# Kernel tuning notes

Hardware: AMD Instinct MI355X
Metric: run time of the kernel (lower is better)

The kernel has to match this reference:

```python
import jax, jax.numpy as jnp
import numpy as np

EPS = 1e-5  # torch BatchNorm1d default eps


def _bn(x, g, b, m, v):
    # x: [B, C, L]; params: [C] (inference-mode BN using running stats)
    scale = g / jnp.sqrt(v + EPS)
    return x * scale[None, :, None] + (b - m * scale)[None, :, None]


def setup_inputs() -> dict:
    key = jax.random.key(0)
    ks = jax.random.split(key, 16)
    B, C, L, I = 32, 256, 4096, 64
    d = {
        "x_a": jax.random.normal(ks[0], (B, C, L), jnp.float32),
        "x_b": jax.random.normal(ks[1], (B, C, L), jnp.float32),
        "x_c": jax.random.normal(ks[2], (B, C, L), jnp.float32),
        "w1": jax.random.normal(ks[3], (4, I, C), jnp.float32) * 0.05,
        "b1": jax.random.normal(ks[4], (4, I), jnp.float32) * 0.05,
        "bn1_g": jax.random.uniform(ks[5], (4, I), jnp.float32, 0.5, 1.5),
        "bn1_b": jax.random.normal(ks[6], (4, I), jnp.float32) * 0.05,
        "bn1_m": jax.random.normal(ks[7], (4, I), jnp.float32) * 0.05,
        "bn1_v": jax.random.uniform(ks[8], (4, I), jnp.float32, 0.5, 1.5),
        "w2": jax.random.normal(ks[9], (4, C, I), jnp.float32) * 0.05,
        "b2": jax.random.normal(ks[10], (4, C), jnp.float32) * 0.05,
        "bn2_g": jax.random.uniform(ks[11], (4, C), jnp.float32, 0.5, 1.5),
        "bn2_b": jax.random.normal(ks[12], (4, C), jnp.float32) * 0.05,
        "bn2_m": jax.random.normal(ks[13], (4, C), jnp.float32) * 0.05,
        "bn2_v": jax.random.uniform(ks[14], (4, C), jnp.float32, 0.5, 1.5),
    }
    return d


def reference(x_a, x_b, x_c, w1, b1, bn1_g, bn1_b, bn1_m, bn1_v,
              w2, b2, bn2_g, bn2_b, bn2_m, bn2_v):
    def att(x, i, global_pool):
        # branch i: conv1x1 -> BN -> ReLU -> conv1x1 -> BN
        h = jnp.mean(x, axis=-1, keepdims=True) if global_pool else x
        h = jnp.einsum('bcl,ic->bil', h, w1[i]) + b1[i][None, :, None]
        h = jax.nn.relu(_bn(h, bn1_g[i], bn1_b[i], bn1_m[i], bn1_v[i]))
        h = jnp.einsum('bil,ci->bcl', h, w2[i]) + b2[i][None, :, None]
        return _bn(h, bn2_g[i], bn2_b[i], bn2_m[i], bn2_v[i])

    x_ab = x_a + x_b
    wei = jax.nn.sigmoid(att(x_ab, 0, False) + att(x_ab, 1, True))  # [B,C,L]
    xo1 = x_a * wei + x_b * (1.0 - wei)

    x_abc = xo1 + x_c
    wei2 = jax.nn.sigmoid(att(x_abc, 2, False) + att(x_abc, 3, True))
    # NOTE: faithful to source: second blend uses (1 - wei), not (1 - wei2)
    xo2 = xo1 * wei2 + x_c * (1.0 - wei)
    return (xo1 + xo2) * 0.5
```

## Files before the change

kernel.cpp:

```cpp
#include <hip/hip_runtime.h>
#include <cstddef>

#define EPS_ 1e-5f


#define OFF_W1T0 0
#define OFF_W2T0 16384
#define OFF_W1T2 32768
#define OFF_W2T2 49152
#define OFF_C1_0 65536
#define OFF_C2_0 65600
#define OFF_C1_2 65856
#define OFF_C2_2 65920
#define OFF_MEANAB 66176
#define OFF_SUMABC 74368
#define OFF_G1 82560
#define OFF_G3 90752
#define OFF_XO1 131072
#define OFF_P 33685504

__global__ __launch_bounds__(256) void k_prep(
    const float* __restrict__ w1, const float* __restrict__ b1,
    const float* __restrict__ bn1g, const float* __restrict__ bn1b,
    const float* __restrict__ bn1m, const float* __restrict__ bn1v,
    const float* __restrict__ w2, const float* __restrict__ b2,
    const float* __restrict__ bn2g, const float* __restrict__ bn2b,
    const float* __restrict__ bn2m, const float* __restrict__ bn2v,
    float* __restrict__ ws)
{
  int idx = blockIdx.x * 256 + threadIdx.x;
  if (idx < 32768) {
    int slot = idx >> 14, r = idx & 16383;
    int br = slot << 1;
    int c = r >> 6, i = r & 63;
    int gi = (br << 6) + i;
    float s1 = bn1g[gi] / sqrtf(bn1v[gi] + EPS_);
    ws[OFF_W1T0 + (slot << 15) + r] = w1[gi * 256 + c] * s1;
  } else if (idx < 65536) {
    int j = idx - 32768;
    int slot = j >> 14, r = j & 16383;
    int br = slot << 1;
    int i = r >> 8, c = r & 255;
    int gc = (br << 8) + c;
    float s2 = bn2g[gc] / sqrtf(bn2v[gc] + EPS_);
    ws[OFF_W2T0 + (slot << 15) + r] = w2[gc * 64 + i] * s2;
  } else if (idx < 65664) {
    int j = idx - 65536;
    int slot = j >> 6, i = j & 63;
    int gi = ((slot << 1) << 6) + i;
    float s1 = bn1g[gi] / sqrtf(bn1v[gi] + EPS_);
    ws[OFF_C1_0 + slot * 320 + i] = bn1b[gi] + s1 * (b1[gi] - bn1m[gi]);
  } else if (idx < 66176) {
    int j = idx - 65664;
    int slot = j >> 8, c = j & 255;
    int gc = ((slot << 1) << 8) + c;
    float s2 = bn2g[gc] / sqrtf(bn2v[gc] + EPS_);
    ws[OFF_C2_0 + slot * 320 + c] = bn2b[gc] + s2 * (b2[gc] - bn2m[gc]);
  } else if (idx < 74368) {
    ws[OFF_SUMABC + (idx - 66176)] = 0.0f;
  }
}

__global__ __launch_bounds__(256) void k_mean_ab(
    const float* __restrict__ xa, const float* __restrict__ xb,
    float* __restrict__ mean_ab)
{
  const int row = blockIdx.x;
  const size_t base4 = (size_t)row * 1024;
  const float4* a4 = (const float4*)xa;
  const float4* b4 = (const float4*)xb;
  float s = 0.0f;
#pragma unroll
  for (int k = 0; k < 4; ++k) {
    float4 va = a4[base4 + k * 256 + threadIdx.x];
    float4 vb = b4[base4 + k * 256 + threadIdx.x];
    s += (va.x + vb.x) + (va.y + vb.y) + (va.z + vb.z) + (va.w + vb.w);
  }
#pragma unroll
  for (int m = 32; m; m >>= 1) s += __shfl_xor(s, m, 64);
  __shared__ float part[4];
  if ((threadIdx.x & 63) == 0) part[threadIdx.x >> 6] = s;
  __syncthreads();
  if (threadIdx.x == 0)
    mean_ab[row] = (part[0] + part[1] + part[2] + part[3]) * (1.0f / 4096.0f);
}

__global__ __launch_bounds__(256) void k_gatt(
    int br, const float* __restrict__ vin, float scale,
    const float* __restrict__ w1, const float* __restrict__ b1,
    const float* __restrict__ bn1g, const float* __restrict__ bn1b,
    const float* __restrict__ bn1m, const float* __restrict__ bn1v,
    const float* __restrict__ w2, const float* __restrict__ b2,
    const float* __restrict__ bn2g, const float* __restrict__ bn2b,
    const float* __restrict__ bn2m, const float* __restrict__ bn2v,
    float* __restrict__ gout)
{
  const int b = blockIdx.x, tid = threadIdx.x;
  __shared__ float xs[256];
  __shared__ float as[64];
  xs[tid] = vin[(b << 8) + tid] * scale;
  __syncthreads();
  if (tid < 64) {
    const int gi = (br << 6) + tid;
    const float* wr = w1 + gi * 256;
    float acc = 0.0f;
#pragma unroll 8
    for (int c = 0; c < 256; ++c) acc = fmaf(wr[c], xs[c], acc);
    float s1 = bn1g[gi] / sqrtf(bn1v[gi] + EPS_);
    float h = s1 * (acc + b1[gi] - bn1m[gi]) + bn1b[gi];
    as[tid] = fmaxf(h, 0.0f);
  }
  __syncthreads();
  const int gc = (br << 8) + tid;
  const float* wr2 = w2 + gc * 64;
  float acc = 0.0f;
#pragma unroll 8
  for (int i = 0; i < 64; ++i) acc = fmaf(wr2[i], as[i], acc);
  float s2 = bn2g[gc] / sqrtf(bn2v[gc] + EPS_);
  gout[(b << 8) + tid] = s2 * (acc + b2[gc] - bn2m[gc]) + bn2b[gc];
}

__global__ __launch_bounds__(256, 4) void k_local1(
    const float* __restrict__ xa, const float* __restrict__ xb,
    const float* __restrict__ xc,
    const float* __restrict__ W1t, const float* __restrict__ W2t,
    const float* __restrict__ c1, const float* __restrict__ c2,
    const float* __restrict__ g1,
    float* __restrict__ xo1, float* __restrict__ pbuf,
    float* __restrict__ sumabc)
{
  const int tid = threadIdx.x;
  const int b = blockIdx.x >> 6;
  const int l0tile = (blockIdx.x & 63) << 6;
  __shared__ float xs[64][64];
  __shared__ float cgs[256];
  const size_t rowbase = ((size_t)b << 20) + (size_t)l0tile;

  cgs[tid] = c2[tid] + g1[(b << 8) + tid];

  const int ti = tid >> 4, i0 = ti << 2;
  const int lt = tid & 15, l0 = lt << 2;
  float acc[4][4] = {};
  const int srow = tid >> 4;
  const int scol = (tid & 15) << 2;

  for (int kb = 0; kb < 4; ++kb) {
    __syncthreads();
#pragma unroll
    for (int pass = 0; pass < 4; ++pass) {
      const int r = (pass << 4) + srow;
      const size_t off = rowbase + (((size_t)(kb << 6) + r) << 12) + scol;
      const float4 va = *(const float4*)(xa + off);
      const float4 vb = *(const float4*)(xb + off);
      float4 v;
      v.x = va.x + vb.x; v.y = va.y + vb.y; v.z = va.z + vb.z; v.w = va.w + vb.w;
      *(float4*)&xs[r][scol] = v;
    }
    __syncthreads();

    const float* wp = W1t + ((kb << 6) << 6) + i0;
#pragma unroll 4
    for (int c = 0; c < 64; ++c) {
      const float4 wv = *(const float4*)(wp + (c << 6));
      const float4 xv = *(const float4*)&xs[c][l0];
      const float wv4[4] = {wv.x, wv.y, wv.z, wv.w};
      const float xv4[4] = {xv.x, xv.y, xv.z, xv.w};
#pragma unroll
      for (int a = 0; a < 4; ++a)
#pragma unroll
        for (int j = 0; j < 4; ++j)
          acc[a][j] = fmaf(wv4[a], xv4[j], acc[a][j]);
    }
  }

  __syncthreads();
#pragma unroll
  for (int a = 0; a < 4; ++a) {
    const float cv = c1[i0 + a];
    float4 h;
    h.x = fmaxf(acc[a][0] + cv, 0.0f);
    h.y = fmaxf(acc[a][1] + cv, 0.0f);
    h.z = fmaxf(acc[a][2] + cv, 0.0f);
    h.w = fmaxf(acc[a][3] + cv, 0.0f);
    *(float4*)&xs[i0 + a][l0] = h;
  }
  __syncthreads();

  const int cg = tid >> 3, c0 = cg << 3;
  const int lt2 = tid & 7, l0b = lt2 << 3;
  float acc2[8][8] = {};
#pragma unroll 2
  for (int i = 0; i < 64; ++i) {
    const float4 h0 = *(const float4*)&xs[i][l0b];
    const float4 h1 = *(const float4*)&xs[i][l0b + 4];
    const float* w2p = W2t + (i << 8) + c0;
    const float4 w0 = *(const float4*)(w2p);
    const float4 w1v = *(const float4*)(w2p + 4);
    const float hh[8] = {h0.x, h0.y, h0.z, h0.w, h1.x, h1.y, h1.z, h1.w};
    const float ww[8] = {w0.x, w0.y, w0.z, w0.w, w1v.x, w1v.y, w1v.z, w1v.w};
#pragma unroll
    for (int a = 0; a < 8; ++a)
#pragma unroll
      for (int j = 0; j < 8; ++j)
        acc2[a][j] = fmaf(ww[a], hh[j], acc2[a][j]);
  }

#pragma unroll
  for (int a = 0; a < 8; ++a) {
    const int cc = c0 + a;
    const float cgv = cgs[cc];
    const size_t off = rowbase + ((size_t)cc << 12) + l0b;
    const float4 a0 = *(const float4*)(xa + off);
    const float4 a1 = *(const float4*)(xa + off + 4);
    const float4 b0 = *(const float4*)(xb + off);
    const float4 b1v = *(const float4*)(xb + off + 4);
    const float4 q0 = *(const float4*)(xc + off);
    const float4 q1 = *(const float4*)(xc + off + 4);
    const float av[8] = {a0.x, a0.y, a0.z, a0.w, a1.x, a1.y, a1.z, a1.w};
    const float bv[8] = {b0.x, b0.y, b0.z, b0.w, b1v.x, b1v.y, b1v.z, b1v.w};
    const float qv[8] = {q0.x, q0.y, q0.z, q0.w, q1.x, q1.y, q1.z, q1.w};
    float ov[8], pv[8], sab = 0.0f;
#pragma unroll
    for (int j = 0; j < 8; ++j) {
      const float w = 1.0f / (1.0f + __expf(-(acc2[a][j] + cgv)));
      const float xo = av[j] * w + bv[j] * (1.0f - w);
      ov[j] = xo;
      pv[j] = 0.5f * (1.0f - w) * qv[j];
      sab += xo + qv[j];
    }
    float4 o0 = {ov[0], ov[1], ov[2], ov[3]}, o1 = {ov[4], ov[5], ov[6], ov[7]};
    float4 p0 = {pv[0], pv[1], pv[2], pv[3]}, p1 = {pv[4], pv[5], pv[6], pv[7]};
    *(float4*)(xo1 + off) = o0;  *(float4*)(xo1 + off + 4) = o1;
    *(float4*)(pbuf + off) = p0; *(float4*)(pbuf + off + 4) = p1;
    sab += __shfl_xor(sab, 1, 64);
    sab += __shfl_xor(sab, 2, 64);
    sab += __shfl_xor(sab, 4, 64);
    if (lt2 == 0) atomicAdd(&sumabc[(b << 8) + cc], sab);
  }
}

__global__ __launch_bounds__(256, 4) void k_local2(
    const float* __restrict__ xo1, const float* __restrict__ xc,
    const float* __restrict__ pbuf,
    const float* __restrict__ W1t, const float* __restrict__ W2t,
    const float* __restrict__ c1, const float* __restrict__ c2,
    const float* __restrict__ g3,
    float* __restrict__ outp)
{
  const int tid = threadIdx.x;
  const int b = blockIdx.x >> 6;
  const int l0tile = (blockIdx.x & 63) << 6;
  __shared__ float xs[64][64];
  __shared__ float cgs[256];
  const size_t rowbase = ((size_t)b << 20) + (size_t)l0tile;

  cgs[tid] = c2[tid] + g3[(b << 8) + tid];

  const int ti = tid >> 4, i0 = ti << 2;
  const int lt = tid & 15, l0 = lt << 2;
  float acc[4][4] = {};
  const int srow = tid >> 4;
  const int scol = (tid & 15) << 2;

  for (int kb = 0; kb < 4; ++kb) {
    __syncthreads();
#pragma unroll
    for (int pass = 0; pass < 4; ++pass) {
      const int r = (pass << 4) + srow;
      const size_t off = rowbase + (((size_t)(kb << 6) + r) << 12) + scol;
      const float4 vo = *(const float4*)(xo1 + off);
      const float4 vq = *(const float4*)(xc + off);
      float4 v;
      v.x = vo.x + vq.x; v.y = vo.y + vq.y; v.z = vo.z + vq.z; v.w = vo.w + vq.w;
      *(float4*)&xs[r][scol] = v;
    }
    __syncthreads();

    const float* wp = W1t + ((kb << 6) << 6) + i0;
#pragma unroll 4
    for (int c = 0; c < 64; ++c) {
      const float4 wv = *(const float4*)(wp + (c << 6));
      const float4 xv = *(const float4*)&xs[c][l0];
      const float wv4[4] = {wv.x, wv.y, wv.z, wv.w};
      const float xv4[4] = {xv.x, xv.y, xv.z, xv.w};
#pragma unroll
      for (int a = 0; a < 4; ++a)
#pragma unroll
        for (int j = 0; j < 4; ++j)
          acc[a][j] = fmaf(wv4[a], xv4[j], acc[a][j]);
    }
  }

  __syncthreads();
#pragma unroll
  for (int a = 0; a < 4; ++a) {
    const float cv = c1[i0 + a];
    float4 h;
    h.x = fmaxf(acc[a][0] + cv, 0.0f);
    h.y = fmaxf(acc[a][1] + cv, 0.0f);
    h.z = fmaxf(acc[a][2] + cv, 0.0f);
    h.w = fmaxf(acc[a][3] + cv, 0.0f);
    *(float4*)&xs[i0 + a][l0] = h;
  }
  __syncthreads();

  const int cg = tid >> 3, c0 = cg << 3;
  const int lt2 = tid & 7, l0b = lt2 << 3;
  float acc2[8][8] = {};
#pragma unroll 2
  for (int i = 0; i < 64; ++i) {
    const float4 h0 = *(const float4*)&xs[i][l0b];
    const float4 h1 = *(const float4*)&xs[i][l0b + 4];
    const float* w2p = W2t + (i << 8) + c0;
    const float4 w0 = *(const float4*)(w2p);
    const float4 w1v = *(const float4*)(w2p + 4);
    const float hh[8] = {h0.x, h0.y, h0.z, h0.w, h1.x, h1.y, h1.z, h1.w};
    const float ww[8] = {w0.x, w0.y, w0.z, w0.w, w1v.x, w1v.y, w1v.z, w1v.w};
#pragma unroll
    for (int a = 0; a < 8; ++a)
#pragma unroll
      for (int j = 0; j < 8; ++j)
        acc2[a][j] = fmaf(ww[a], hh[j], acc2[a][j]);
  }

#pragma unroll
  for (int a = 0; a < 8; ++a) {
    const int cc = c0 + a;
    const float cgv = cgs[cc];
    const size_t off = rowbase + ((size_t)cc << 12) + l0b;
    const float4 o0g = *(const float4*)(xo1 + off);
    const float4 o1g = *(const float4*)(xo1 + off + 4);
    const float4 p0 = *(const float4*)(pbuf + off);
    const float4 p1 = *(const float4*)(pbuf + off + 4);
    const float xov[8] = {o0g.x, o0g.y, o0g.z, o0g.w, o1g.x, o1g.y, o1g.z, o1g.w};
    const float pv[8] = {p0.x, p0.y, p0.z, p0.w, p1.x, p1.y, p1.z, p1.w};
    float ov[8];
#pragma unroll
    for (int j = 0; j < 8; ++j) {
      const float w2s = 1.0f / (1.0f + __expf(-(acc2[a][j] + cgv)));
      ov[j] = 0.5f * xov[j] * (1.0f + w2s) + pv[j];
    }
    float4 r0 = {ov[0], ov[1], ov[2], ov[3]}, r1 = {ov[4], ov[5], ov[6], ov[7]};
    *(float4*)(outp + off) = r0;
    *(float4*)(outp + off + 4) = r1;
  }
}

extern "C" void kernel_launch(void* const* d_in, const int* in_sizes, int n_in,
                              void* d_out, int out_size, void* d_ws, size_t ws_size,
                              hipStream_t stream) {
  const float* xa = (const float*)d_in[0];
  const float* xb = (const float*)d_in[1];
  const float* xc = (const float*)d_in[2];
  const float* w1 = (const float*)d_in[3];
  const float* b1 = (const float*)d_in[4];
  const float* bn1g = (const float*)d_in[5];
  const float* bn1b = (const float*)d_in[6];
  const float* bn1m = (const float*)d_in[7];
  const float* bn1v = (const float*)d_in[8];
  const float* w2 = (const float*)d_in[9];
  const float* b2 = (const float*)d_in[10];
  const float* bn2g = (const float*)d_in[11];
  const float* bn2b = (const float*)d_in[12];
  const float* bn2m = (const float*)d_in[13];
  const float* bn2v = (const float*)d_in[14];
  float* ws = (float*)d_ws;
  float* outp = (float*)d_out;

  float* W1t0 = ws + OFF_W1T0;
  float* W2t0 = ws + OFF_W2T0;
  float* W1t2 = ws + OFF_W1T2;
  float* W2t2 = ws + OFF_W2T2;
  float* c1_0 = ws + OFF_C1_0;
  float* c2_0 = ws + OFF_C2_0;
  float* c1_2 = ws + OFF_C1_2;
  float* c2_2 = ws + OFF_C2_2;
  float* mean_ab = ws + OFF_MEANAB;
  float* sum_abc = ws + OFF_SUMABC;
  float* g1 = ws + OFF_G1;
  float* g3 = ws + OFF_G3;
  float* xo1 = ws + OFF_XO1;
  float* pbuf = ws + OFF_P;

  k_prep<<<291, 256, 0, stream>>>(w1, b1, bn1g, bn1b, bn1m, bn1v,
                                  w2, b2, bn2g, bn2b, bn2m, bn2v, ws);
  k_mean_ab<<<8192, 256, 0, stream>>>(xa, xb, mean_ab);
  k_gatt<<<32, 256, 0, stream>>>(1, mean_ab, 1.0f,
                                 w1, b1, bn1g, bn1b, bn1m, bn1v,
                                 w2, b2, bn2g, bn2b, bn2m, bn2v, g1);
  k_local1<<<2048, 256, 0, stream>>>(xa, xb, xc, W1t0, W2t0, c1_0, c2_0, g1,
                                     xo1, pbuf, sum_abc);
  k_gatt<<<32, 256, 0, stream>>>(3, sum_abc, 1.0f / 4096.0f,
                                 w1, b1, bn1g, bn1b, bn1m, bn1v,
                                 w2, b2, bn2g, bn2b, bn2m, bn2v, g3);
  k_local2<<<2048, 256, 0, stream>>>(xo1, xc, pbuf, W1t2, W2t2, c1_2, c2_2, g3,
                                     outp);
}
```

Measured before the change: 827.6 us.

## Restructure local kernels to 512 threads with wave-uniform weights and double-buffered input tiles

The two local attention kernels now launch 512 threads, with each wavefront owning a slice of output channels. Weight reads use a wave-uniform index (readfirstlane), so they can become scalar loads while each lane handles one spatial position. The input tile is double-buffered in shared memory, and the next chunk is prefetched into registers while the current one is computed. The epilogue switches from float4 accesses to scalar per-lane coalesced accesses, and the atomic partial sums use a full-wave reduction. In exchange, the kernels use more shared memory and more registers (32 accumulators per lane), and the global traffic uses narrower accesses.

```diff
diff --git a/kernel.cpp b/kernel.cpp
--- a/kernel.cpp
+++ b/kernel.cpp
@@ -120,7 +120,7 @@
   gout[(b << 8) + tid] = s2 * (acc + b2[gc] - bn2m[gc]) + bn2b[gc];
 }
 
-__global__ __launch_bounds__(256, 4) void k_local1(
+__global__ __launch_bounds__(512, 6) void k_local1(
     const float* __restrict__ xa, const float* __restrict__ xb,
     const float* __restrict__ xc,
     const float* __restrict__ W1t, const float* __restrict__ W2t,
@@ -130,116 +130,99 @@
     float* __restrict__ sumabc)
 {
   const int tid = threadIdx.x;
+  const int lane = tid & 63;
+  const int wav = __builtin_amdgcn_readfirstlane(tid >> 6);
   const int b = blockIdx.x >> 6;
-  const int l0tile = (blockIdx.x & 63) << 6;
-  __shared__ float xs[64][64];
+  const int l0 = (blockIdx.x & 63) << 6;
+  __shared__ float xs[2][64][64];
+  __shared__ float hs[64][64];
   __shared__ float cgs[256];
-  const size_t rowbase = ((size_t)b << 20) + (size_t)l0tile;
-
-  cgs[tid] = c2[tid] + g1[(b << 8) + tid];
-
-  const int ti = tid >> 4, i0 = ti << 2;
-  const int lt = tid & 15, l0 = lt << 2;
-  float acc[4][4] = {};
+  const size_t rowbase = ((size_t)b << 20) + (size_t)l0;
+
+  if (tid < 256) cgs[tid] = c2[tid] + g1[(b << 8) + tid];
+
   const int srow = tid >> 4;
   const int scol = (tid & 15) << 2;
 
+  float4 ra0, rb0, ra1, rb1;
+  {
+    const size_t o0 = rowbase + ((size_t)srow << 12) + scol;
+    const size_t o1 = rowbase + ((size_t)(srow + 32) << 12) + scol;
+    ra0 = *(const float4*)(xa + o0); rb0 = *(const float4*)(xb + o0);
+    ra1 = *(const float4*)(xa + o1); rb1 = *(const float4*)(xb + o1);
+  }
+  {
+    float4 v0 = {ra0.x + rb0.x, ra0.y + rb0.y, ra0.z + rb0.z, ra0.w + rb0.w};
+    float4 v1 = {ra1.x + rb1.x, ra1.y + rb1.y, ra1.z + rb1.z, ra1.w + rb1.w};
+    *(float4*)&xs[0][srow][scol] = v0;
+    *(float4*)&xs[0][srow + 32][scol] = v1;
+  }
+  __syncthreads();
+
+  const int i0 = wav << 3;
+  float acc[8] = {0.f, 0.f, 0.f, 0.f, 0.f, 0.f, 0.f, 0.f};
+  const float* __restrict__ w1base = W1t + i0;
   for (int kb = 0; kb < 4; ++kb) {
+    if (kb < 3) {
+      const size_t cb = rowbase + ((size_t)((kb + 1) << 6) << 12);
+      const size_t o0 = cb + ((size_t)srow << 12) + scol;
+      const size_t o1 = cb + ((size_t)(srow + 32) << 12) + scol;
+      ra0 = *(const float4*)(xa + o0); rb0 = *(const float4*)(xb + o0);
+      ra1 = *(const float4*)(xa + o1); rb1 = *(const float4*)(xb + o1);
+    }
+    const float* __restrict__ wr0 = w1base + ((kb << 6) << 6);
+    const int pb = kb & 1;
+#pragma unroll 2
+    for (int c = 0; c < 64; ++c) {
+      const float xv = xs[pb][c][lane];
+      const float* wr = wr0 + (c << 6);
+#pragma unroll
+      for (int i = 0; i < 8; ++i) acc[i] = fmaf(wr[i], xv, acc[i]);
+    }
     __syncthreads();
-#pragma unroll
-    for (int pass = 0; pass < 4; ++pass) {
-      const int r = (pass << 4) + srow;
-      const size_t off = rowbase + (((size_t)(kb << 6) + r) << 12) + scol;
-      const float4 va = *(const float4*)(xa + off);
-      const float4 vb = *(const float4*)(xb + off);
-      float4 v;
-      v.x = va.x + vb.x; v.y = va.y + vb.y; v.z = va.z + vb.z; v.w = va.w + vb.w;
-      *(float4*)&xs[r][scol] = v;
-    }
-    __syncthreads();
-
-    const float* wp = W1t + ((kb << 6) << 6) + i0;
-#pragma unroll 4
-    for (int c = 0; c < 64; ++c) {
-      const float4 wv = *(const float4*)(wp + (c << 6));
-      const float4 xv = *(const float4*)&xs[c][l0];
-      const float wv4[4] = {wv.x, wv.y, wv.z, wv.w};
-      const float xv4[4] = {xv.x, xv.y, xv.z, xv.w};
-#pragma unroll
-      for (int a = 0; a < 4; ++a)
-#pragma unroll
-        for (int j = 0; j < 4; ++j)
-          acc[a][j] = fmaf(wv4[a], xv4[j], acc[a][j]);
-    }
-  }
-
-  __syncthreads();
-#pragma unroll
-  for (int a = 0; a < 4; ++a) {
-    const float cv = c1[i0 + a];
-    float4 h;
-    h.x = fmaxf(acc[a][0] + cv, 0.0f);
-    h.y = fmaxf(acc[a][1] + cv, 0.0f);
-    h.z = fmaxf(acc[a][2] + cv, 0.0f);
-    h.w = fmaxf(acc[a][3] + cv, 0.0f);
-    *(float4*)&xs[i0 + a][l0] = h;
-  }
-  __syncthreads();
-
-  const int cg = tid >> 3, c0 = cg << 3;
-  const int lt2 = tid & 7, l0b = lt2 << 3;
-  float acc2[8][8] = {};
-#pragma unroll 2
-  for (int i = 0; i < 64; ++i) {
-    const float4 h0 = *(const float4*)&xs[i][l0b];
-    const float4 h1 = *(const float4*)&xs[i][l0b + 4];
-    const float* w2p = W2t + (i << 8) + c0;
-    const float4 w0 = *(const float4*)(w2p);
-    const float4 w1v = *(const float4*)(w2p + 4);
-    const float hh[8] = {h0.x, h0.y, h0.z, h0.w, h1.x, h1.y, h1.z, h1.w};
-    const float ww[8] = {w0.x, w0.y, w0.z, w0.w, w1v.x, w1v.y, w1v.z, w1v.w};
-#pragma unroll
-    for (int a = 0; a < 8; ++a)
-#pragma unroll
-      for (int j = 0; j < 8; ++j)
-        acc2[a][j] = fmaf(ww[a], hh[j], acc2[a][j]);
-  }
-
-#pragma unroll
-  for (int a = 0; a < 8; ++a) {
-    const int cc = c0 + a;
-    const float cgv = cgs[cc];
-    const size_t off = rowbase + ((size_t)cc << 12) + l0b;
-    const float4 a0 = *(const float4*)(xa + off);
-    const float4 a1 = *(const float4*)(xa + off + 4);
-    const float4 b0 = *(const float4*)(xb + off);
-    const float4 b1v = *(const float4*)(xb + off + 4);
-    const float4 q0 = *(const float4*)(xc + off);
-    const float4 q1 = *(const float4*)(xc + off + 4);
-    const float av[8] = {a0.x, a0.y, a0.z, a0.w, a1.x, a1.y, a1.z, a1.w};
-    const float bv[8] = {b0.x, b0.y, b0.z, b0.w, b1v.x, b1v.y, b1v.z, b1v.w};
-    const float qv[8] = {q0.x, q0.y, q0.z, q0.w, q1.x, q1.y, q1.z, q1.w};
-    float ov[8], pv[8], sab = 0.0f;
-#pragma unroll
-    for (int j = 0; j < 8; ++j) {
-      const float w = 1.0f / (1.0f + __expf(-(acc2[a][j] + cgv)));
-      const float xo = av[j] * w + bv[j] * (1.0f - w);
-      ov[j] = xo;
-      pv[j] = 0.5f * (1.0f - w) * qv[j];
-      sab += xo + qv[j];
-    }
-    float4 o0 = {ov[0], ov[1], ov[2], ov[3]}, o1 = {ov[4], ov[5], ov[6], ov[7]};
-    float4 p0 = {pv[0], pv[1], pv[2], pv[3]}, p1 = {pv[4], pv[5], pv[6], pv[7]};
-    *(float4*)(xo1 + off) = o0;  *(float4*)(xo1 + off + 4) = o1;
-    *(float4*)(pbuf + off) = p0; *(float4*)(pbuf + off + 4) = p1;
-    sab += __shfl_xor(sab, 1, 64);
-    sab += __shfl_xor(sab, 2, 64);
-    sab += __shfl_xor(sab, 4, 64);
-    if (lt2 == 0) atomicAdd(&sumabc[(b << 8) + cc], sab);
-  }
-}
-
-__global__ __launch_bounds__(256, 4) void k_local2(
+    if (kb < 3) {
+      const int nb = (kb + 1) & 1;
+      float4 v0 = {ra0.x + rb0.x, ra0.y + rb0.y, ra0.z + rb0.z, ra0.w + rb0.w};
+      float4 v1 = {ra1.x + rb1.x, ra1.y + rb1.y, ra1.z + rb1.z, ra1.w + rb1.w};
+      *(float4*)&xs[nb][srow][scol] = v0;
+      *(float4*)&xs[nb][srow + 32][scol] = v1;
+      __syncthreads();
+    }
+  }
+
+#pragma unroll
+  for (int i = 0; i < 8; ++i)
+    hs[i0 + i][lane] = fmaxf(acc[i] + c1[i0 + i], 0.0f);
+  __syncthreads();
+
+  const int cc0 = wav << 5;
+  float acc2[32];
+#pragma unroll
+  for (int j = 0; j < 32; ++j) acc2[j] = 0.0f;
+  const float* __restrict__ w2base = W2t + cc0;
+  for (int ii = 0; ii < 64; ++ii) {
+    const float hv = hs[ii][lane];
+    const float* wr = w2base + (ii << 8);
+#pragma unroll
+    for (int j = 0; j < 32; ++j) acc2[j] = fmaf(wr[j], hv, acc2[j]);
+  }
+
+  for (int j = 0; j < 32; ++j) {
+    const int cc = cc0 + j;
+    const size_t off = rowbase + ((size_t)cc << 12) + (size_t)lane;
+    const float w = 1.0f / (1.0f + __expf(-(acc2[j] + cgs[cc])));
+    const float a = xa[off], bb = xb[off], q = xc[off];
+    const float xo = fmaf(a - bb, w, bb);
+    xo1[off] = xo;
+    pbuf[off] = 0.5f * (1.0f - w) * q;
+    float s = xo + q;
+#pragma unroll
+    for (int m = 1; m < 64; m <<= 1) s += __shfl_xor(s, m, 64);
+    if (lane == 0) atomicAdd(&sumabc[(b << 8) + cc], s);
+  }
+}
+
+__global__ __launch_bounds__(512, 6) void k_local2(
     const float* __restrict__ xo1, const float* __restrict__ xc,
     const float* __restrict__ pbuf,
     const float* __restrict__ W1t, const float* __restrict__ W2t,
@@ -248,101 +231,90 @@
     float* __restrict__ outp)
 {
   const int tid = threadIdx.x;
+  const int lane = tid & 63;
+  const int wav = __builtin_amdgcn_readfirstlane(tid >> 6);
   const int b = blockIdx.x >> 6;
-  const int l0tile = (blockIdx.x & 63) << 6;
-  __shared__ float xs[64][64];
+  const int l0 = (blockIdx.x & 63) << 6;
+  __shared__ float xs[2][64][64];
+  __shared__ float hs[64][64];
   __shared__ float cgs[256];
-  const size_t rowbase = ((size_t)b << 20) + (size_t)l0tile;
-
-  cgs[tid] = c2[tid] + g3[(b << 8) + tid];
-
-  const int ti = tid >> 4, i0 = ti << 2;
-  const int lt = tid & 15, l0 = lt << 2;
-  float acc[4][4] = {};
+  const size_t rowbase = ((size_t)b << 20) + (size_t)l0;
+
+  if (tid < 256) cgs[tid] = c2[tid] + g3[(b << 8) + tid];
+
   const int srow = tid >> 4;
   const int scol = (tid & 15) << 2;
 
+  float4 ra0, rb0, ra1, rb1;
+  {
+    const size_t o0 = rowbase + ((size_t)srow << 12) + scol;
+    const size_t o1 = rowbase + ((size_t)(srow + 32) << 12) + scol;
+    ra0 = *(const float4*)(xo1 + o0); rb0 = *(const float4*)(xc + o0);
+    ra1 = *(const float4*)(xo1 + o1); rb1 = *(const float4*)(xc + o1);
+  }
+  {
+    float4 v0 = {ra0.x + rb0.x, ra0.y + rb0.y, ra0.z + rb0.z, ra0.w + rb0.w};
+    float4 v1 = {ra1.x + rb1.x, ra1.y + rb1.y, ra1.z + rb1.z, ra1.w + rb1.w};
+    *(float4*)&xs[0][srow][scol] = v0;
+    *(float4*)&xs[0][srow + 32][scol] = v1;
+  }
+  __syncthreads();
+
+  const int i0 = wav << 3;
+  float acc[8] = {0.f, 0.f, 0.f, 0.f, 0.f, 0.f, 0.f, 0.f};
+  const float* __restrict__ w1base = W1t + i0;
   for (int kb = 0; kb < 4; ++kb) {
+    if (kb < 3) {
+      const size_t cb = rowbase + ((size_t)((kb + 1) << 6) << 12);
+      const size_t o0 = cb + ((size_t)srow << 12) + scol;
+      const size_t o1 = cb + ((size_t)(srow + 32) << 12) + scol;
+      ra0 = *(const float4*)(xo1 + o0); rb0 = *(const float4*)(xc + o0);
+      ra1 = *(const float4*)(xo1 + o1); rb1 = *(const float4*)(xc + o1);
+    }
+    const float* __restrict__ wr0 = w1base + ((kb << 6) << 6);
+    const int pb = kb & 1;
+#pragma unroll 2
+    for (int c = 0; c < 64; ++c) {
+      const float xv = xs[pb][c][lane];
+      const float* wr = wr0 + (c << 6);
+#pragma unroll
+      for (int i = 0; i < 8; ++i) acc[i] = fmaf(wr[i], xv, acc[i]);
+    }
     __syncthreads();
-#pragma unroll
-    for (int pass = 0; pass < 4; ++pass) {
-      const int r = (pass << 4) + srow;
-      const size_t off = rowbase + (((size_t)(kb << 6) + r) << 12) + scol;
-      const float4 vo = *(const float4*)(xo1 + off);
-      const float4 vq = *(const float4*)(xc + off);
-      float4 v;
-      v.x = vo.x + vq.x; v.y = vo.y + vq.y; v.z = vo.z + vq.z; v.w = vo.w + vq.w;
-      *(float4*)&xs[r][scol] = v;
-    }
-    __syncthreads();
-
-    const float* wp = W1t + ((kb << 6) << 6) + i0;
-#pragma unroll 4
-    for (int c = 0; c < 64; ++c) {
-      const float4 wv = *(const float4*)(wp + (c << 6));
-      const float4 xv = *(const float4*)&xs[c][l0];
-      const float wv4[4] = {wv.x, wv.y, wv.z, wv.w};
-      const float xv4[4] = {xv.x, xv.y, xv.z, xv.w};
-#pragma unroll
-      for (int a = 0; a < 4; ++a)
-#pragma unroll
-        for (int j = 0; j < 4; ++j)
-          acc[a][j] = fmaf(wv4[a], xv4[j], acc[a][j]);
-    }
-  }
-
-  __syncthreads();
-#pragma unroll
-  for (int a = 0; a < 4; ++a) {
-    const float cv = c1[i0 + a];
-    float4 h;
-    h.x = fmaxf(acc[a][0] + cv, 0.0f);
-    h.y = fmaxf(acc[a][1] + cv, 0.0f);
-    h.z = fmaxf(acc[a][2] + cv, 0.0f);
-    h.w = fmaxf(acc[a][3] + cv, 0.0f);
-    *(float4*)&xs[i0 + a][l0] = h;
-  }
-  __syncthreads();
-
-  const int cg = tid >> 3, c0 = cg << 3;
-  const int lt2 = tid & 7, l0b = lt2 << 3;
-  float acc2[8][8] = {};
-#pragma unroll 2
-  for (int i = 0; i < 64; ++i) {
-    const float4 h0 = *(const float4*)&xs[i][l0b];
-    const float4 h1 = *(const float4*)&xs[i][l0b + 4];
-    const float* w2p = W2t + (i << 8) + c0;
-    const float4 w0 = *(const float4*)(w2p);
-    const float4 w1v = *(const float4*)(w2p + 4);
-    const float hh[8] = {h0.x, h0.y, h0.z, h0.w, h1.x, h1.y, h1.z, h1.w};
-    const float ww[8] = {w0.x, w0.y, w0.z, w0.w, w1v.x, w1v.y, w1v.z, w1v.w};
-#pragma unroll
-    for (int a = 0; a < 8; ++a)
-#pragma unroll
-      for (int j = 0; j < 8; ++j)
-        acc2[a][j] = fmaf(ww[a], hh[j], acc2[a][j]);
-  }
-
-#pragma unroll
-  for (int a = 0; a < 8; ++a) {
-    const int cc = c0 + a;
-    const float cgv = cgs[cc];
-    const size_t off = rowbase + ((size_t)cc << 12) + l0b;
-    const float4 o0g = *(const float4*)(xo1 + off);
-    const float4 o1g = *(const float4*)(xo1 + off + 4);
-    const float4 p0 = *(const float4*)(pbuf + off);
-    const float4 p1 = *(const float4*)(pbuf + off + 4);
-    const float xov[8] = {o0g.x, o0g.y, o0g.z, o0g.w, o1g.x, o1g.y, o1g.z, o1g.w};
-    const float pv[8] = {p0.x, p0.y, p0.z, p0.w, p1.x, p1.y, p1.z, p1.w};
-    float ov[8];
-#pragma unroll
-    for (int j = 0; j < 8; ++j) {
-      const float w2s = 1.0f / (1.0f + __expf(-(acc2[a][j] + cgv)));
-      ov[j] = 0.5f * xov[j] * (1.0f + w2s) + pv[j];
-    }
-    float4 r0 = {ov[0], ov[1], ov[2], ov[3]}, r1 = {ov[4], ov[5], ov[6], ov[7]};
-    *(float4*)(outp + off) = r0;
-    *(float4*)(outp + off + 4) = r1;
+    if (kb < 3) {
+      const int nb = (kb + 1) & 1;
+      float4 v0 = {ra0.x + rb0.x, ra0.y + rb0.y, ra0.z + rb0.z, ra0.w + rb0.w};
+      float4 v1 = {ra1.x + rb1.x, ra1.y + rb1.y, ra1.z + rb1.z, ra1.w + rb1.w};
+      *(float4*)&xs[nb][srow][scol] = v0;
+      *(float4*)&xs[nb][srow + 32][scol] = v1;
+      __syncthreads();
+    }
+  }
+
+#pragma unroll
+  for (int i = 0; i < 8; ++i)
+    hs[i0 + i][lane] = fmaxf(acc[i] + c1[i0 + i], 0.0f);
+  __syncthreads();
+
+  const int cc0 = wav << 5;
+  float acc2[32];
+#pragma unroll
+  for (int j = 0; j < 32; ++j) acc2[j] = 0.0f;
+  const float* __restrict__ w2base = W2t + cc0;
+  for (int ii = 0; ii < 64; ++ii) {
+    const float hv = hs[ii][lane];
+    const float* wr = w2base + (ii << 8);
+#pragma unroll
+    for (int j = 0; j < 32; ++j) acc2[j] = fmaf(wr[j], hv, acc2[j]);
+  }
+
+  for (int j = 0; j < 32; ++j) {
+    const int cc = cc0 + j;
+    const size_t off = rowbase + ((size_t)cc << 12) + (size_t)lane;
+    const float w2s = 1.0f / (1.0f + __expf(-(acc2[j] + cgs[cc])));
+    const float xov = xo1[off];
+    const float pv = pbuf[off];
+    outp[off] = fmaf(0.5f * xov, w2s, fmaf(0.5f, xov, pv));
   }
 }
 
@@ -388,11 +360,11 @@
   k_gatt<<<32, 256, 0, stream>>>(1, mean_ab, 1.0f,
                                  w1, b1, bn1g, bn1b, bn1m, bn1v,
                                  w2, b2, bn2g, bn2b, bn2m, bn2v, g1);
-  k_local1<<<2048, 256, 0, stream>>>(xa, xb, xc, W1t0, W2t0, c1_0, c2_0, g1,
+  k_local1<<<2048, 512, 0, stream>>>(xa, xb, xc, W1t0, W2t0, c1_0, c2_0, g1,
                                      xo1, pbuf, sum_abc);
   k_gatt<<<32, 256, 0, stream>>>(3, sum_abc, 1.0f / 4096.0f,
                                  w1, b1, bn1g, bn1b, bn1m, bn1v,
                                  w2, b2, bn2g, bn2b, bn2m, bn2v, g3);
-  k_local2<<<2048, 256, 0, stream>>>(xo1, xc, pbuf, W1t2, W2t2, c1_2, c2_2, g3,
+  k_local2<<<2048, 512, 0, stream>>>(xo1, xc, pbuf, W1t2, W2t2, c1_2, c2_2, g3,
                                      outp);
 }
```

Measured after the change: 911.3 us. +10.1%, slower.
